# Kernel optimization log

Hardware: AMD Instinct MI355X
Metric: run time of the kernel (lower is better)

## Reference

```python
import jax, jax.numpy as jnp
import numpy as np

K = 32  # knn neighborhood size (hard-coded in get_graph_feature)
EPS_BN = 1e-5


def _bn(x, g, b):
    # batch-norm (training-mode batch stats) over all axes except the last (channel) axis
    axes = tuple(range(x.ndim - 1))
    m = jnp.mean(x, axis=axes, keepdims=True)
    v = jnp.var(x, axis=axes, keepdims=True)
    return (x - m) * jax.lax.rsqrt(v + EPS_BN) * g + b


def _knn_idx(xt, k):
    # xt: [B, N, C] -> indices of k nearest points [B, N, k] (torch topk on -||xi-xj||^2)
    xx = jnp.sum(xt * xt, axis=-1)                       # [B, N]
    inner = jnp.einsum('bnc,bmc->bnm', xt, xt)           # [B, N, N]
    neg_d2 = -(xx[:, :, None] - 2.0 * inner + xx[:, None, :])
    _, idx = jax.lax.top_k(neg_d2, k)
    return idx


def _graph_feature(x, k=K):
    # x: [B, C, N] -> feature [B, N, k, 2C] matching torch cat((neighbors, center))
    xt = jnp.transpose(x, (0, 2, 1))                     # [B, N, C]
    idx = _knn_idx(xt, k)                                # [B, N, k]
    gathered = jax.vmap(lambda a, i: a[i])(xt, idx)      # [B, N, k, C]
    center = jnp.broadcast_to(xt[:, :, None, :], gathered.shape)
    return jnp.concatenate([gathered, center], axis=-1)


def _dgcnn(x, w1, w2, w3, w4, w5, g1, g2, g3, g4, g5, b1, b2, b3, b4, b5):
    # x: [B, 3, N] -> embeddings [B, emb, N]
    feat = _graph_feature(x)                                         # [B, N, K, 6]
    h = jax.nn.relu(_bn(jnp.einsum('bnkc,oc->bnko', feat, w1), g1, b1))
    x1 = jnp.max(h, axis=2)                                          # [B, N, 64]
    h = jax.nn.relu(_bn(jnp.einsum('bnkc,oc->bnko', h, w2), g2, b2))
    x2 = jnp.max(h, axis=2)
    h = jax.nn.relu(_bn(jnp.einsum('bnkc,oc->bnko', h, w3), g3, b3))
    x3 = jnp.max(h, axis=2)
    h = jax.nn.relu(_bn(jnp.einsum('bnkc,oc->bnko', h, w4), g4, b4))
    x4 = jnp.max(h, axis=2)
    cat = jnp.concatenate([x1, x2, x3, x4], axis=-1)                 # [B, N, 512]
    emb = jax.nn.relu(_bn(jnp.einsum('bnc,oc->bno', cat, w5), g5, b5))
    return jnp.transpose(emb, (0, 2, 1))                             # [B, emb, N]


def _pairwise_distance_batch(x, y):
    # x: [B, c, N], y: [B, c, M] -> euclidean distances [B, N, M] (faithful incl. clamp/mask)
    xx = jnp.sum(x * x, axis=1)                          # [B, N]
    yy = jnp.sum(y * y, axis=1)                          # [B, M]
    inner = jnp.einsum('bcn,bcm->bnm', x, y)
    pd = xx[:, :, None] - 2.0 * inner + yy[:, None, :]
    pd_sq = jnp.where(pd > 0.0, pd, 0.0)
    err = (pd_sq <= 0.0).astype(pd.dtype)
    d = jnp.sqrt(pd_sq + err * 1e-16)
    return d * (1.0 - err)


def setup_inputs() -> dict:
    key = jax.random.key(0)
    ks = jax.random.split(key, 20)
    B, N = 4, 2048
    def w(k, o, i):
        return jax.random.normal(k, (o, i), jnp.float32) * (1.0 / np.sqrt(i))
    inp = {
        'src': jax.random.normal(ks[0], (B, 3, N), jnp.float32),
        'tgt': jax.random.normal(ks[1], (B, 3, N), jnp.float32),
        'w1': w(ks[2], 64, 6), 'w2': w(ks[3], 64, 64), 'w3': w(ks[4], 128, 64),
        'w4': w(ks[5], 256, 128), 'w5': w(ks[6], 512, 512),
        'g1': jnp.ones(64), 'g2': jnp.ones(64), 'g3': jnp.ones(128),
        'g4': jnp.ones(256), 'g5': jnp.ones(512),
        'b1': jnp.zeros(64), 'b2': jnp.zeros(64), 'b3': jnp.zeros(128),
        'b4': jnp.zeros(256), 'b5': jnp.zeros(512),
    }
    return inp


def reference(src, tgt, w1, w2, w3, w4, w5, g1, g2, g3, g4, g5, b1, b2, b3, b4, b5):
    params = (w1, w2, w3, w4, w5, g1, g2, g3, g4, g5, b1, b2, b3, b4, b5)
    f_src = _dgcnn(src, *params)                         # [B, emb, N]
    f_tgt = _dgcnn(tgt, *params)                         # [B, emb, N] (siamese)
    d = _pairwise_distance_batch(f_src, f_tgt)           # [B, N, M]
    scores = jax.nn.softmax(-d, axis=-1)                 # soft correspondence
    src_corr = jnp.einsum('bcm,bnm->bcn', tgt, scores)   # tgt @ scores^T, [B, 3, N]
    return src_corr
```

## Files before the change

kernel.cpp:

```cpp
#include <hip/hip_runtime.h>
#include <hip/hip_bf16.h>
#include <math.h>

#define BB 4
#define NN 2048
#define KK 32
#define GG 2
constexpr int BNr = BB * NN;
constexpr int SGr = BB * NN * KK;
constexpr int SR  = GG * SGr;

typedef __hip_bfloat16 bf16;
typedef __attribute__((ext_vector_type(8))) short bf16x8;
typedef __attribute__((ext_vector_type(4))) short s16x4;
typedef __attribute__((ext_vector_type(4))) float f32x4;
__device__ __forceinline__ float b2f(bf16 v) { return __bfloat162float(v); }
__device__ __forceinline__ bf16  f2b(float v) { return __float2bfloat16(v); }
__device__ __forceinline__ short f2bs(float v) { bf16 b = f2b(v); return *(short*)&b; }
__device__ __forceinline__ float bs2f(short s) { bf16 b; *(short*)&b = s; return b2f(b); }

#define SWZ128(b) ((b) ^ ((((b) >> 7) & 7) << 4))
#define SWZ256(b) ((b) ^ ((((b) >> 8) & 7) << 4))

__global__ __launch_bounds__(256) void knn_kernel(const float* __restrict__ src,
                                                  const float* __restrict__ tgt,
                                                  int* __restrict__ idx_out) {
    __shared__ float pts[3 * NN];
    __shared__ float xxs[NN];
    int blk = blockIdx.x;
    int gb = blk >> 9;
    int chunk = blk & 511;
    int g = gb >> 2, b = gb & 3;
    const float* x = (g == 0 ? src : tgt) + (size_t)b * 3 * NN;
    int t = threadIdx.x;
    for (int i = t; i < 3 * NN; i += 256) pts[i] = x[i];
    __syncthreads();
    for (int m = t; m < NN; m += 256) {
        float p0 = pts[m], p1 = pts[NN + m], p2 = pts[2 * NN + m];
        xxs[m] = p0 * p0 + p1 * p1 + p2 * p2;
    }
    __syncthreads();
    int w = t >> 6, l = t & 63;
    int n = chunk * 4 + w;
    float q0 = pts[n], q1 = pts[NN + n], q2 = pts[2 * NN + n];
    float xxn = xxs[n];
    float d2[32];
#pragma unroll
    for (int s = 0; s < 32; ++s) {
        int m = s * 64 + l;
        float dot = q0 * pts[m] + q1 * pts[NN + m] + q2 * pts[2 * NN + m];
        d2[s] = (xxn - 2.0f * dot) + xxs[m];
    }
    float gval[4]; int gslot[4];
#pragma unroll
    for (int G = 0; G < 4; ++G) {
        float v = d2[G * 8]; int sl = G * 8;
#pragma unroll
        for (int s = 1; s < 8; ++s)
            if (d2[G * 8 + s] < v) { v = d2[G * 8 + s]; sl = G * 8 + s; }
        gval[G] = v; gslot[G] = sl;
    }
    int* outp = idx_out + ((size_t)gb * NN + n) * KK;
    for (int k = 0; k < KK; ++k) {
        float bv = fminf(fminf(gval[0], gval[1]), fminf(gval[2], gval[3]));
        float gv = bv;
#pragma unroll
        for (int off = 1; off < 64; off <<= 1) gv = fminf(gv, __shfl_xor(gv, off));
        unsigned long long mask = __ballot(bv == gv);
        int winner = (int)__builtin_ctzll(mask);
        if (l == winner) {
            int grp = (gval[0] == gv) ? 0 : (gval[1] == gv) ? 1 : (gval[2] == gv) ? 2 : 3;
#pragma unroll
            for (int G = 0; G < 4; ++G)
                if (G == grp) {
                    int bs = gslot[G];
                    outp[k] = bs * 64 + l;
#pragma unroll
                    for (int s = 0; s < 8; ++s)
                        if (G * 8 + s == bs) d2[G * 8 + s] = INFINITY;
                    float v = d2[G * 8]; int sl = G * 8;
#pragma unroll
                    for (int s = 1; s < 8; ++s)
                        if (d2[G * 8 + s] < v) { v = d2[G * 8 + s]; sl = G * 8 + s; }
                    gval[G] = v; gslot[G] = sl;
                }
        }
    }
}

__global__ void zero_kernel(float* __restrict__ p, int n) {
    int i = blockIdx.x * 256 + threadIdx.x;
    if (i < n) p[i] = 0.f;
}

__global__ void cvt_all_kernel(const float* __restrict__ w2, const float* __restrict__ w3,
                               const float* __restrict__ w4, const float* __restrict__ w5,
                               bf16* __restrict__ w2b, bf16* __restrict__ w3b,
                               bf16* __restrict__ w4b, bf16* __restrict__ w5b) {
    int i = blockIdx.x * 256 + threadIdx.x;
    if (i < 4096)   w2b[i] = f2b(w2[i]);
    if (i < 8192)   w3b[i] = f2b(w3[i]);
    if (i < 32768)  w4b[i] = f2b(w4[i]);
    if (i < 262144) w5b[i] = f2b(w5[i]);
}

__global__ void finalize_bn_kernel(float* __restrict__ sums, int C,
                                   const float* __restrict__ gamma,
                                   const float* __restrict__ beta,
                                   float cnt, float* __restrict__ params) {
    int i = blockIdx.x * blockDim.x + threadIdx.x;
    if (i >= GG * C) return;
    int g = i / C, c = i - g * C;
    float s  = sums[(g * 512 + c) * 2 + 0];
    float sq = sums[(g * 512 + c) * 2 + 1];
    float mean = s / cnt;
    float var = sq / cnt - mean * mean;
    if (var < 0.f) var = 0.f;
    float sc = gamma[c] * rsqrtf(var + 1e-5f);
    params[(g * 512 + c) * 2 + 0] = sc;
    params[(g * 512 + c) * 2 + 1] = beta[c] - mean * sc;
    sums[(g * 512 + c) * 2 + 0] = 0.f;
    sums[(g * 512 + c) * 2 + 1] = 0.f;
}

template <int MODE>
__global__ __launch_bounds__(256, 3) void l12_mfma(
    const float* __restrict__ src, const float* __restrict__ tgt,
    const float* __restrict__ w1, const bf16* __restrict__ w2b,
    const int* __restrict__ idx, const float* __restrict__ p1,
    bf16* __restrict__ H2, bf16* __restrict__ cat, float* __restrict__ sums) {
    __shared__ char F1s[32768];
    __shared__ char W2s[8192];
    __shared__ float epiA[512];
    __shared__ float epiB[128];
    int tid = threadIdx.x;
    int w = tid >> 6, l = tid & 63, lg = l >> 4, lr = l & 15;
    long long row0 = (long long)blockIdx.x * 256;
    int g = (int)(row0 / SGr);

    epiA[tid] = 0.f; epiA[tid + 256] = 0.f;
    if (MODE == 1) {
        if (tid < 128) epiB[tid] = 0.f;
        for (int s = tid; s < 512; s += 256)
            *(bf16x8*)(W2s + SWZ128(s * 16)) = *(const bf16x8*)(w2b + s * 8);
    }

    bf16x8 af[4];
#pragma unroll
    for (int i = 0; i < 4; ++i) {
        af[i] = (bf16x8){0, 0, 0, 0, 0, 0, 0, 0};
        if (lg == 0) {
            int rr = (int)row0 + w * 64 + 16 * i + lr;
            int nrow = rr >> 5;
            int n = nrow & (NN - 1);
            int gb = nrow >> 11;
            int b = gb & 3, gg = gb >> 2;
            const float* x = (gg ? tgt : src) + (size_t)b * 3 * NN;
            int j = idx[rr];
            af[i][0] = f2bs(x[j]);
            af[i][1] = f2bs(x[NN + j]);
            af[i][2] = f2bs(x[2 * NN + j]);
            af[i][3] = f2bs(x[n]);
            af[i][4] = f2bs(x[NN + n]);
            af[i][5] = f2bs(x[2 * NN + n]);
        }
    }
    bf16x8 bf1[4];
#pragma unroll
    for (int j = 0; j < 4; ++j) {
        bf1[j] = (bf16x8){0, 0, 0, 0, 0, 0, 0, 0};
        if (lg == 0) {
            int o = 16 * j + lr;
#pragma unroll
            for (int c = 0; c < 6; ++c) bf1[j][c] = f2bs(w1[o * 6 + c]);
        }
    }

    f32x4 acc1[4][4] = {};
#pragma unroll
    for (int i = 0; i < 4; ++i)
#pragma unroll
        for (int j = 0; j < 4; ++j)
            acc1[i][j] = __builtin_amdgcn_mfma_f32_16x16x32_bf16(af[i], bf1[j], acc1[i][j], 0, 0, 0);

    __syncthreads();

    if (MODE == 0) {
#pragma unroll
        for (int j = 0; j < 4; ++j) {
            int c = 16 * j + lr;
            float s = 0.f, q = 0.f;
#pragma unroll
            for (int i = 0; i < 4; ++i)
#pragma unroll
                for (int r = 0; r < 4; ++r) { float v = acc1[i][j][r]; s += v; q += v * v; }
            s += __shfl_xor(s, 16); s += __shfl_xor(s, 32);
            q += __shfl_xor(q, 16); q += __shfl_xor(q, 32);
            if (lg == 0) {
                atomicAdd(&epiA[c * 2], s);
                atomicAdd(&epiA[c * 2 + 1], q);
            }
        }
        __syncthreads();
        if (tid < 128) atomicAdd(&sums[g * 1024 + tid], epiA[tid]);
        return;
    }

#pragma unroll
    for (int j = 0; j < 4; ++j) {
        int c = 16 * j + lr;
        float sc = p1[(g * 512 + c) * 2], sh = p1[(g * 512 + c) * 2 + 1];
#pragma unroll
        for (int i = 0; i < 4; ++i) {
            float m = 0.f;
#pragma unroll
            for (int r = 0; r < 4; ++r) {
                float v = fmaf(acc1[i][j][r], sc, sh);
                v = v > 0.f ? v : 0.f;
                m = fmaxf(m, v);
                int rowi = w * 64 + 16 * i + 4 * lg + r;
                *(bf16*)(F1s + SWZ128((rowi * 64 + c) * 2)) = f2b(v);
            }
            int p = 2 * w + (i >> 1);
            atomicMax((int*)epiA + p * 64 + c, __float_as_int(m));
        }
    }
    __syncthreads();

    {
        long long pt0 = row0 >> 5;
        for (int e = tid; e < 512; e += 256) {
            int p = e >> 6, c = e & 63;
            cat[(pt0 + p) * 512 + c] = f2b(__int_as_float(((int*)epiA)[p * 64 + c]));
        }
    }

    f32x4 acc2[4][4] = {};
#pragma unroll
    for (int ks = 0; ks < 2; ++ks) {
        bf16x8 bv[4];
#pragma unroll
        for (int j = 0; j < 4; ++j)
            bv[j] = *(bf16x8*)(W2s + SWZ128(((16 * j + lr) * 64 + ks * 32 + lg * 8) * 2));
#pragma unroll
        for (int i = 0; i < 4; ++i) {
            bf16x8 a = *(bf16x8*)(F1s + SWZ128(((w * 64 + 16 * i + lr) * 64 + ks * 32 + lg * 8) * 2));
#pragma unroll
            for (int j = 0; j < 4; ++j)
                acc2[i][j] = __builtin_amdgcn_mfma_f32_16x16x32_bf16(a, bv[j], acc2[i][j], 0, 0, 0);
        }
    }

#pragma unroll
    for (int j = 0; j < 4; ++j) {
        int c = 16 * j + lr;
        float s = 0.f, q = 0.f;
#pragma unroll
        for (int i = 0; i < 4; ++i)
#pragma unroll
            for (int r = 0; r < 4; ++r) {
                float v = acc2[i][j][r];
                s += v; q += v * v;
                long long gr = row0 + w * 64 + 16 * i + 4 * lg + r;
                H2[gr * 64 + c] = f2b(v);
            }
        s += __shfl_xor(s, 16); s += __shfl_xor(s, 32);
        q += __shfl_xor(q, 16); q += __shfl_xor(q, 32);
        if (lg == 0) {
            atomicAdd(&epiB[c * 2], s);
            atomicAdd(&epiB[c * 2 + 1], q);
        }
    }
    __syncthreads();
    if (tid < 128) atomicAdd(&sums[g * 1024 + tid], epiB[tid]);
}

template <int APPLY>
__global__ __launch_bounds__(512, 2) void chain34_mfma(
    const bf16* __restrict__ H2, const bf16* __restrict__ w3b,
    const bf16* __restrict__ w4b, const float* __restrict__ p2,
    const float* __restrict__ p3, const float* __restrict__ p4,
    bf16* __restrict__ cat, float* __restrict__ sums) {
    extern __shared__ char smem[];
    char* W3s = smem;
    char* W4s = smem + 16384;
    char* A2s = smem + 81920;
    char* F3s = smem + 98304;
    float* P3s = (float*)(smem + 131072);
    float* P4s = (float*)(smem + 132096);
    float* epi = (float*)(smem + 134144);
    float* P2s = (float*)(smem + 138240);

    int tid = threadIdx.x;
    int w = tid >> 6, l = tid & 63, lg = l >> 4, lr = l & 15;
    long long rowB0 = (long long)blockIdx.x * 512;
    int g = (int)(rowB0 / SGr);

    for (int s = tid; s < 1024; s += 512)
        *(bf16x8*)(W3s + SWZ128(s * 16)) = *(const bf16x8*)(w3b + s * 8);
    for (int s = tid; s < 4096; s += 512)
        *(bf16x8*)(W4s + SWZ256(s * 16)) = *(const bf16x8*)(w4b + s * 8);
    if (tid < 256) P3s[tid] = p3[g * 1024 + tid];
    if (tid < 128) P2s[tid] = p2[g * 1024 + tid];
    P4s[tid] = p4 ? p4[g * 1024 + tid] : 0.f;
    if (!APPLY) epi[tid] = 0.f;
    __syncthreads();

    float sc3[4], sh3[4];
#pragma unroll
    for (int r = 0; r < 4; ++r) {
        int c = 16 * w + 4 * lg + r;
        sc3[r] = P3s[c * 2]; sh3[r] = P3s[c * 2 + 1];
    }

    for (int chunk = 0; chunk < 4; ++chunk) {
        long long row0 = rowB0 + chunk * 128;
        for (int s = tid; s < 1024; s += 512) {
            bf16x8 rv = *(const bf16x8*)(H2 + row0 * 64 + s * 8);
            int cb = (s & 7) * 8;
            bf16x8 ov;
#pragma unroll
            for (int e = 0; e < 8; ++e) {
                float v = fmaf(bs2f(rv[e]), P2s[(cb + e) * 2], P2s[(cb + e) * 2 + 1]);
                v = v > 0.f ? v : 0.f;
                ov[e] = f2bs(v);
            }
            *(bf16x8*)(A2s + SWZ128(s * 16)) = ov;
        }
        if (APPLY) { ((int*)epi)[tid] = 0; ((int*)epi)[tid + 512] = 0; }
        __syncthreads();

        {
            f32x4 acc3[8] = {};
#pragma unroll
            for (int ks = 0; ks < 2; ++ks) {
                bf16x8 wf = *(bf16x8*)(W3s + SWZ128(((16 * w + lr) * 64 + ks * 32 + lg * 8) * 2));
#pragma unroll
                for (int j = 0; j < 8; ++j) {
                    bf16x8 a2 = *(bf16x8*)(A2s + SWZ128(((16 * j + lr) * 64 + ks * 32 + lg * 8) * 2));
                    acc3[j] = __builtin_amdgcn_mfma_f32_16x16x32_bf16(wf, a2, acc3[j], 0, 0, 0);
                }
            }
#pragma unroll
            for (int j = 0; j < 8; ++j) {
                s16x4 pk;
#pragma unroll
                for (int r = 0; r < 4; ++r) {
                    float v = fmaf(acc3[j][r], sc3[r], sh3[r]);
                    v = v > 0.f ? v : 0.f;
                    pk[r] = f2bs(v);
                }
                *(s16x4*)(F3s + SWZ256(((16 * j + lr) * 128 + 16 * w + 4 * lg) * 2)) = pk;
            }
        }
        __syncthreads();

        f32x4 acc4[16] = {};
#pragma unroll
        for (int ks = 0; ks < 4; ++ks) {
            bf16x8 a = *(bf16x8*)(F3s + SWZ256(((16 * w + lr) * 128 + ks * 32 + lg * 8) * 2));
#pragma unroll
            for (int j = 0; j < 16; ++j) {
                bf16x8 b = *(bf16x8*)(W4s + SWZ256(((16 * j + lr) * 128 + ks * 32 + lg * 8) * 2));
                acc4[j] = __builtin_amdgcn_mfma_f32_16x16x32_bf16(a, b, acc4[j], 0, 0, 0);
            }
        }

        if (!APPLY) {
#pragma unroll
            for (int j = 0; j < 16; ++j) {
                int c = 16 * j + lr;
                float s = acc4[j][0] + acc4[j][1] + acc4[j][2] + acc4[j][3];
                float q = acc4[j][0] * acc4[j][0] + acc4[j][1] * acc4[j][1] +
                          acc4[j][2] * acc4[j][2] + acc4[j][3] * acc4[j][3];
                s += __shfl_xor(s, 16); s += __shfl_xor(s, 32);
                q += __shfl_xor(q, 16); q += __shfl_xor(q, 32);
                if (lg == 0) {
                    atomicAdd(&epi[c * 2], s);
                    atomicAdd(&epi[c * 2 + 1], q);
                }
            }
        } else {
#pragma unroll
            for (int j = 0; j < 16; ++j) {
                int c = 16 * j + lr;
                float sc = P4s[c * 2], sh = P4s[c * 2 + 1];
                float m = 0.f;
#pragma unroll
                for (int r = 0; r < 4; ++r) {
                    float v = fmaf(acc4[j][r], sc, sh);
                    v = v > 0.f ? v : 0.f;
                    m = fmaxf(m, v);
                }
                m = fmaxf(m, __shfl_xor(m, 16));
                m = fmaxf(m, __shfl_xor(m, 32));
                if (lg == 0)
                    atomicMax((int*)epi + (w >> 1) * 256 + c, __float_as_int(m));
            }
            __syncthreads();
            long long pt0 = row0 >> 5;
            for (int e = tid; e < 1024; e += 512) {
                int p = e >> 8, c = e & 255;
                cat[(pt0 + p) * 512 + 256 + c] = f2b(__int_as_float(((int*)epi)[p * 256 + c]));
            }
            {
                int p = tid >> 7, c = tid & 127;
                float m = 0.f;
                for (int r = 0; r < 32; ++r)
                    m = fmaxf(m, b2f(*(bf16*)(F3s + SWZ256(((p * 32 + r) * 128 + c) * 2))));
                cat[(pt0 + p) * 512 + 128 + c] = f2b(m);
            }
        }
        __syncthreads();
    }
    if (!APPLY) {
        atomicAdd(&sums[g * 1024 + tid], epi[tid]);
    }
}

template <int MODE, int CH, int BNA>
__global__ __launch_bounds__(256, 4) void mfma_gemm(
    const bf16* __restrict__ A, const bf16* __restrict__ Wt,
    float* __restrict__ OutF, bf16* __restrict__ OutB,
    int Cin, int ldOut, long long sA, long long sW, long long sO,
    int rowsPerGroup, const float* __restrict__ params, float* __restrict__ sums,
    const float* __restrict__ pba, bf16* __restrict__ cat) {
    __shared__ char As[16384];
    __shared__ char Bs[8192];
    __shared__ float epi[128];
    __shared__ float PBs[128];
    __shared__ int x2m[256];
    int tid = threadIdx.x;
    int w = tid >> 6, l = tid & 63, lg = l >> 4, lr = l & 15;
    int bz = blockIdx.z;
    const bf16* Ap = A + (long long)bz * sA;
    const bf16* Wp = Wt + (long long)bz * sW;
    int o0 = blockIdx.y * 64;
    long long rowB0 = (long long)blockIdx.x * (128 * CH);
    int g = (int)(rowB0 / rowsPerGroup);
    if ((MODE == 1 || MODE == 3) && tid < 128) epi[tid] = 0.f;
    if (BNA && tid < 128) PBs[tid] = pba[g * 1024 + tid];
    int wr = (w >> 1) * 64, wc = (w & 1) * 32;

    for (int ch = 0; ch < CH; ++ch) {
        long long row0 = rowB0 + (long long)ch * 128;
        if (BNA) {
            __syncthreads();
            if (tid < 256) x2m[tid] = 0;
        }
        f32x4 acc[4][2] = {};
        for (int k0 = 0; k0 < Cin; k0 += 64) {
            __syncthreads();
            for (int s = tid; s < 1024; s += 256) {
                if (BNA) {
                    bf16x8 rv = *(const bf16x8*)(Ap + (row0 + (s >> 3)) * Cin + k0 + (s & 7) * 8);
                    int cb = k0 + (s & 7) * 8;
                    int pt = (s >> 3) >> 5;
                    bf16x8 ov;
#pragma unroll
                    for (int e = 0; e < 8; ++e) {
                        float v = fmaf(bs2f(rv[e]), PBs[(cb + e) * 2], PBs[(cb + e) * 2 + 1]);
                        v = v > 0.f ? v : 0.f;
                        ov[e] = f2bs(v);
                        atomicMax(&x2m[pt * 64 + cb + e], __float_as_int(v));
                    }
                    *(bf16x8*)(As + SWZ128(s * 16)) = ov;
                } else {
                    *(bf16x8*)(As + SWZ128(s * 16)) =
                        *(const bf16x8*)(Ap + (row0 + (s >> 3)) * Cin + k0 + (s & 7) * 8);
                }
            }
            for (int s = tid; s < 512; s += 256)
                *(bf16x8*)(Bs + SWZ128(s * 16)) =
                    *(const bf16x8*)(Wp + (long long)(o0 + (s >> 3)) * Cin + k0 + (s & 7) * 8);
            __syncthreads();
#pragma unroll
            for (int ks = 0; ks < 2; ++ks) {
                bf16x8 b0 = *(bf16x8*)(Bs + SWZ128(((wc + lr) * 64 + ks * 32 + lg * 8) * 2));
                bf16x8 b1 = *(bf16x8*)(Bs + SWZ128(((wc + 16 + lr) * 64 + ks * 32 + lg * 8) * 2));
#pragma unroll
                for (int i = 0; i < 4; ++i) {
                    bf16x8 a = *(bf16x8*)(As + SWZ128(((wr + 16 * i + lr) * 64 + ks * 32 + lg * 8) * 2));
                    acc[i][0] = __builtin_amdgcn_mfma_f32_16x16x32_bf16(a, b0, acc[i][0], 0, 0, 0);
                    acc[i][1] = __builtin_amdgcn_mfma_f32_16x16x32_bf16(a, b1, acc[i][1], 0, 0, 0);
                }
            }
        }
        if (BNA && blockIdx.y == 0) {
            long long pt0 = row0 >> 5;
            if (tid < 256) {
                int p = tid >> 6, c = tid & 63;
                cat[(pt0 + p) * 512 + 64 + c] = f2b(__int_as_float(x2m[tid]));
            }
        }
        if (MODE == 1 || MODE == 3) {
#pragma unroll
            for (int j = 0; j < 2; ++j) {
                int c = wc + 16 * j + lr;
                float s = 0.f, q = 0.f;
#pragma unroll
                for (int i = 0; i < 4; ++i)
#pragma unroll
                    for (int r = 0; r < 4; ++r) {
                        float v = acc[i][j][r];
                        s += v; q += v * v;
                    }
                s += __shfl_xor(s, 16); s += __shfl_xor(s, 32);
                q += __shfl_xor(q, 16); q += __shfl_xor(q, 32);
                if (lg == 0) {
                    atomicAdd(&epi[c * 2], s);
                    atomicAdd(&epi[c * 2 + 1], q);
                }
            }
        }
        if (MODE == 0 || MODE == 3) {
            float* Op = OutF + (long long)bz * sO;
#pragma unroll
            for (int j = 0; j < 2; ++j) {
                int gc = o0 + wc + 16 * j + lr;
#pragma unroll
                for (int i = 0; i < 4; ++i)
#pragma unroll
                    for (int r = 0; r < 4; ++r) {
                        long long gr = row0 + wr + 16 * i + 4 * lg + r;
                        Op[gr * ldOut + gc] = acc[i][j][r];
                    }
            }
        }
    }
    if (MODE == 1 || MODE == 3) {
        __syncthreads();
        if (tid < 128) atomicAdd(&sums[g * 1024 + o0 * 2 + tid], epi[tid]);
    }
}

__global__ __launch_bounds__(256) void emb_finalize(const float* __restrict__ h5,
                                                    const float* __restrict__ p5,
                                                    bf16* __restrict__ embB,
                                                    float* __restrict__ nrm) {
    __shared__ float red[256];
    int row = blockIdx.x; int t = threadIdx.x;
    int g = row / BNr;
    float s = 0.f;
#pragma unroll
    for (int i = 0; i < 2; ++i) {
        int c = t + i * 256;
        float v = fmaf(h5[(size_t)row * 512 + c], p5[(g * 512 + c) * 2], p5[(g * 512 + c) * 2 + 1]);
        v = v > 0.f ? v : 0.f;
        bf16 bb = f2b(v);
        embB[(size_t)row * 512 + c] = bb;
        float vb = b2f(bb);
        s += vb * vb;
    }
    red[t] = s; __syncthreads();
    for (int st = 128; st > 0; st >>= 1) { if (t < st) red[t] += red[t + st]; __syncthreads(); }
    if (t == 0) nrm[row] = red[0];
}

__global__ __launch_bounds__(256) void corr_kernel(const float* __restrict__ inner,
                                                   const float* __restrict__ nrm,
                                                   const float* __restrict__ tgt,
                                                   float* __restrict__ out) {
    __shared__ float red[256];
    int blk = blockIdx.x;
    int b = blk >> 11, n = blk & (NN - 1);
    int t = threadIdx.x;
    const float* inr = inner + ((size_t)b * NN + n) * NN;
    float xx = nrm[b * NN + n];
    float dloc[8];
    float vmax = -INFINITY;
#pragma unroll
    for (int i = 0; i < 8; ++i) {
        int m = t + i * 256;
        float pd = (xx - 2.f * inr[m]) + nrm[BNr + b * NN + m];
        float d = pd > 0.f ? sqrtf(pd) : 0.f;
        dloc[i] = d;
        vmax = fmaxf(vmax, -d);
    }
    red[t] = vmax; __syncthreads();
    for (int s = 128; s > 0; s >>= 1) { if (t < s) red[t] = fmaxf(red[t], red[t + s]); __syncthreads(); }
    vmax = red[0]; __syncthreads();
    const float* tp = tgt + (size_t)b * 3 * NN;
    float se = 0.f, s0 = 0.f, s1 = 0.f, s2 = 0.f;
#pragma unroll
    for (int i = 0; i < 8; ++i) {
        int m = t + i * 256;
        float p = expf(-dloc[i] - vmax);
        se += p;
        s0 += p * tp[m]; s1 += p * tp[NN + m]; s2 += p * tp[2 * NN + m];
    }
    red[t] = se; __syncthreads();
    for (int s = 128; s > 0; s >>= 1) { if (t < s) red[t] += red[t + s]; __syncthreads(); }
    float tot = red[0]; __syncthreads();
    red[t] = s0; __syncthreads();
    for (int s = 128; s > 0; s >>= 1) { if (t < s) red[t] += red[t + s]; __syncthreads(); }
    float o0v = red[0]; __syncthreads();
    red[t] = s1; __syncthreads();
    for (int s = 128; s > 0; s >>= 1) { if (t < s) red[t] += red[t + s]; __syncthreads(); }
    float o1v = red[0]; __syncthreads();
    red[t] = s2; __syncthreads();
    for (int s = 128; s > 0; s >>= 1) { if (t < s) red[t] += red[t + s]; __syncthreads(); }
    float o2v = red[0];
    if (t == 0) {
        out[(size_t)b * 3 * NN + n]          = o0v / tot;
        out[(size_t)b * 3 * NN + NN + n]     = o1v / tot;
        out[(size_t)b * 3 * NN + 2 * NN + n] = o2v / tot;
    }
}

extern "C" void kernel_launch(void* const* d_in, const int* in_sizes, int n_in,
                              void* d_out, int out_size, void* d_ws, size_t ws_size,
                              hipStream_t stream) {
    const float* src = (const float*)d_in[0];
    const float* tgt = (const float*)d_in[1];
    const float* w1  = (const float*)d_in[2];
    const float* w2  = (const float*)d_in[3];
    const float* w3  = (const float*)d_in[4];
    const float* w4  = (const float*)d_in[5];
    const float* w5  = (const float*)d_in[6];
    const float* g1  = (const float*)d_in[7];
    const float* g2  = (const float*)d_in[8];
    const float* g3  = (const float*)d_in[9];
    const float* g4  = (const float*)d_in[10];
    const float* g5  = (const float*)d_in[11];
    const float* b1  = (const float*)d_in[12];
    const float* b2  = (const float*)d_in[13];
    const float* b3  = (const float*)d_in[14];
    const float* b4  = (const float*)d_in[15];
    const float* b5  = (const float*)d_in[16];
    float* out = (float*)d_out;
    char* ws = (char*)d_ws;
    (void)in_sizes; (void)n_in;

    size_t off = 0;
    auto alloc = [&](size_t bytes) { size_t o = off; off = (off + bytes + 255) & ~(size_t)255; return o; };
    int*   idx  = (int*)(ws + alloc((size_t)SR * 4));
    bf16*  H2   = (bf16*)(ws + alloc((size_t)SR * 64 * 2));
    bf16*  cat  = (bf16*)(ws + alloc((size_t)GG * BNr * 512 * 2));
    bf16*  embB = (bf16*)(ws + alloc((size_t)GG * BNr * 512 * 2));
    float* h5   = (float*)(ws + alloc((size_t)GG * BNr * 512 * 4));
    float* nrm  = (float*)(ws + alloc((size_t)GG * BNr * 4));
    float* sums = (float*)(ws + alloc(2048 * 4));
    float* prm  = (float*)(ws + alloc(5 * 2048 * 4));
    bf16*  w2b  = (bf16*)(ws + alloc(4096 * 2));
    bf16*  w3b  = (bf16*)(ws + alloc(8192 * 2));
    bf16*  w4b  = (bf16*)(ws + alloc(32768 * 2));
    bf16*  w5b  = (bf16*)(ws + alloc(262144 * 2));
    float* P1 = prm, *P2 = prm + 2048, *P3 = prm + 4096, *P4 = prm + 6144, *P5 = prm + 8192;
    float* inner = (float*)H2;

    if (ws_size < off) {
        hipMemsetAsync(d_out, 0, (size_t)out_size * 4, stream);
        return;
    }

    knn_kernel<<<GG * BB * NN / 4, 256, 0, stream>>>(src, tgt, idx);
    cvt_all_kernel<<<1024, 256, 0, stream>>>(w2, w3, w4, w5, w2b, w3b, w4b, w5b);
    zero_kernel<<<8, 256, 0, stream>>>(sums, 2048);

    l12_mfma<0><<<SR / 256, 256, 0, stream>>>(src, tgt, w1, w2b, idx, nullptr, nullptr, nullptr, sums);
    finalize_bn_kernel<<<1, 128, 0, stream>>>(sums, 64, g1, b1, (float)SGr, P1);

    l12_mfma<1><<<SR / 256, 256, 0, stream>>>(src, tgt, w1, w2b, idx, P1, H2, cat, sums);
    finalize_bn_kernel<<<1, 128, 0, stream>>>(sums, 64, g2, b2, (float)SGr, P2);

    mfma_gemm<1, 4, 1><<<dim3(SR / 512, 2, 1), 256, 0, stream>>>(
        H2, w3b, nullptr, nullptr, 64, 0, 0, 0, 0, SGr, nullptr, sums, P2, cat);
    finalize_bn_kernel<<<2, 128, 0, stream>>>(sums, 128, g3, b3, (float)SGr, P3);

    chain34_mfma<0><<<1024, 512, 138752, stream>>>(H2, w3b, w4b, P2, P3, nullptr, nullptr, sums);
    finalize_bn_kernel<<<4, 128, 0, stream>>>(sums, 256, g4, b4, (float)SGr, P4);
    chain34_mfma<1><<<1024, 512, 138752, stream>>>(H2, w3b, w4b, P2, P3, P4, cat, nullptr);

    mfma_gemm<3, 1, 0><<<dim3(GG * BNr / 128, 8, 1), 256, 0, stream>>>(
        cat, w5b, h5, nullptr, 512, 512, 0, 0, 0, BNr, nullptr, sums, nullptr, nullptr);
    finalize_bn_kernel<<<8, 128, 0, stream>>>(sums, 512, g5, b5, (float)BNr, P5);
    emb_finalize<<<GG * BNr, 256, 0, stream>>>(h5, P5, embB, nrm);

    mfma_gemm<0, 1, 0><<<dim3(NN / 128, NN / 64, BB), 256, 0, stream>>>(
        embB, embB + (size_t)BNr * 512, inner, nullptr, 512, 2048,
        (long long)NN * 512, (long long)NN * 512, (long long)NN * NN,
        SGr, nullptr, nullptr, nullptr, nullptr);

    corr_kernel<<<BB * NN, 256, 0, stream>>>(inner, nrm, tgt, out);
}
```

Baseline: 697.8 us.

## Compute layer-1 BN stats from input moments in knn; pipeline chain34 loads

Layer-1 BN statistics are now built analytically: the knn kernel accumulates a 27-entry second-moment matrix of the neighbour and centre coordinates, and a new finalize kernel turns it into the per-channel mean and variance through w1. This removes a full l12_mfma pass over all SR rows. chain34 is also restructured: the next H2 chunk is prefetched into registers, the W4/F3 operand roles are swapped so statistics and max reductions stay in registers instead of going through shared-memory atomics, and the epilogue is simplified. The risks are fp32 cancellation in the moment-based variance and extra atomics at the end of knn.

```diff
diff --git a/kernel.cpp b/kernel.cpp
--- a/kernel.cpp
+++ b/kernel.cpp
@@ -24,15 +24,19 @@
 
 __global__ __launch_bounds__(256) void knn_kernel(const float* __restrict__ src,
                                                   const float* __restrict__ tgt,
-                                                  int* __restrict__ idx_out) {
+                                                  int* __restrict__ idx_out,
+                                                  float* __restrict__ g1s) {
     __shared__ float pts[3 * NN];
     __shared__ float xxs[NN];
+    __shared__ int   sel[4][32];
+    __shared__ float Gs[27];
     int blk = blockIdx.x;
     int gb = blk >> 9;
     int chunk = blk & 511;
     int g = gb >> 2, b = gb & 3;
     const float* x = (g == 0 ? src : tgt) + (size_t)b * 3 * NN;
     int t = threadIdx.x;
+    if (t < 27) Gs[t] = 0.f;
     for (int i = t; i < 3 * NN; i += 256) pts[i] = x[i];
     __syncthreads();
     for (int m = t; m < NN; m += 256) {
@@ -75,6 +79,7 @@
                 if (G == grp) {
                     int bs = gslot[G];
                     outp[k] = bs * 64 + l;
+                    sel[w][k] = bs * 64 + l;
 #pragma unroll
                     for (int s = 0; s < 8; ++s)
                         if (G * 8 + s == bs) d2[G * 8 + s] = INFINITY;
@@ -86,6 +91,42 @@
                 }
         }
     }
+    __syncthreads();
+    float nx = 0.f, ny = 0.f, nz = 0.f;
+    if (l < 32) {
+        int m = sel[w][l];
+        nx = pts[m]; ny = pts[NN + m]; nz = pts[2 * NN + m];
+    }
+    float v9[9] = {nx * nx, nx * ny, nx * nz, ny * ny, ny * nz, nz * nz, nx, ny, nz};
+#pragma unroll
+    for (int e = 0; e < 9; ++e) {
+#pragma unroll
+        for (int off = 1; off < 64; off <<= 1) v9[e] += __shfl_xor(v9[e], off);
+    }
+    if (l == 0) {
+        float c3[3] = {q0, q1, q2};
+#pragma unroll
+        for (int e = 0; e < 6; ++e) atomicAdd(&Gs[e], v9[e]);
+#pragma unroll
+        for (int a = 0; a < 3; ++a)
+#pragma unroll
+            for (int bb = 0; bb < 3; ++bb)
+                atomicAdd(&Gs[6 + a * 3 + bb], v9[6 + a] * c3[bb]);
+        atomicAdd(&Gs[15], 32.f * q0 * q0);
+        atomicAdd(&Gs[16], 32.f * q0 * q1);
+        atomicAdd(&Gs[17], 32.f * q0 * q2);
+        atomicAdd(&Gs[18], 32.f * q1 * q1);
+        atomicAdd(&Gs[19], 32.f * q1 * q2);
+        atomicAdd(&Gs[20], 32.f * q2 * q2);
+        atomicAdd(&Gs[21], v9[6]);
+        atomicAdd(&Gs[22], v9[7]);
+        atomicAdd(&Gs[23], v9[8]);
+        atomicAdd(&Gs[24], 32.f * q0);
+        atomicAdd(&Gs[25], 32.f * q1);
+        atomicAdd(&Gs[26], 32.f * q2);
+    }
+    __syncthreads();
+    if (t < 27) atomicAdd(&g1s[g * 27 + t], Gs[t]);
 }
 
 __global__ void zero_kernel(float* __restrict__ p, int n) {
@@ -123,7 +164,36 @@
     sums[(g * 512 + c) * 2 + 1] = 0.f;
 }
 
-template <int MODE>
+__global__ void finalize_l1_kernel(const float* __restrict__ g1s,
+                                   const float* __restrict__ w1,
+                                   const float* __restrict__ gamma,
+                                   const float* __restrict__ beta,
+                                   float cnt, float* __restrict__ params) {
+    int i = blockIdx.x * blockDim.x + threadIdx.x;
+    if (i >= GG * 64) return;
+    int g = i >> 6, o = i & 63;
+    const float* G = g1s + g * 27;
+    float wv[6];
+#pragma unroll
+    for (int c = 0; c < 6; ++c) wv[c] = w1[o * 6 + c];
+    float s = wv[0] * G[21] + wv[1] * G[22] + wv[2] * G[23] +
+              wv[3] * G[24] + wv[4] * G[25] + wv[5] * G[26];
+    const int UT[6][6] = {{0, 1, 2, 6, 7, 8},   {1, 3, 4, 9, 10, 11},
+                          {2, 4, 5, 12, 13, 14},{6, 9, 12, 15, 16, 17},
+                          {7, 10, 13, 16, 18, 19},{8, 11, 14, 17, 19, 20}};
+    float q = 0.f;
+#pragma unroll
+    for (int a = 0; a < 6; ++a)
+#pragma unroll
+        for (int bb = 0; bb < 6; ++bb) q += wv[a] * wv[bb] * G[UT[a][bb]];
+    float mean = s / cnt;
+    float var = q / cnt - mean * mean;
+    if (var < 0.f) var = 0.f;
+    float sc = gamma[o] * rsqrtf(var + 1e-5f);
+    params[(g * 512 + o) * 2 + 0] = sc;
+    params[(g * 512 + o) * 2 + 1] = beta[o] - mean * sc;
+}
+
 __global__ __launch_bounds__(256, 3) void l12_mfma(
     const float* __restrict__ src, const float* __restrict__ tgt,
     const float* __restrict__ w1, const bf16* __restrict__ w2b,
@@ -139,11 +209,9 @@
     int g = (int)(row0 / SGr);
 
     epiA[tid] = 0.f; epiA[tid + 256] = 0.f;
-    if (MODE == 1) {
-        if (tid < 128) epiB[tid] = 0.f;
-        for (int s = tid; s < 512; s += 256)
-            *(bf16x8*)(W2s + SWZ128(s * 16)) = *(const bf16x8*)(w2b + s * 8);
-    }
+    if (tid < 128) epiB[tid] = 0.f;
+    for (int s = tid; s < 512; s += 256)
+        *(bf16x8*)(W2s + SWZ128(s * 16)) = *(const bf16x8*)(w2b + s * 8);
 
     bf16x8 af[4];
 #pragma unroll
@@ -185,27 +253,6 @@
 
     __syncthreads();
 
-    if (MODE == 0) {
-#pragma unroll
-        for (int j = 0; j < 4; ++j) {
-            int c = 16 * j + lr;
-            float s = 0.f, q = 0.f;
-#pragma unroll
-            for (int i = 0; i < 4; ++i)
-#pragma unroll
-                for (int r = 0; r < 4; ++r) { float v = acc1[i][j][r]; s += v; q += v * v; }
-            s += __shfl_xor(s, 16); s += __shfl_xor(s, 32);
-            q += __shfl_xor(q, 16); q += __shfl_xor(q, 32);
-            if (lg == 0) {
-                atomicAdd(&epiA[c * 2], s);
-                atomicAdd(&epiA[c * 2 + 1], q);
-            }
-        }
-        __syncthreads();
-        if (tid < 128) atomicAdd(&sums[g * 1024 + tid], epiA[tid]);
-        return;
-    }
-
 #pragma unroll
     for (int j = 0; j < 4; ++j) {
         int c = 16 * j + lr;
@@ -303,7 +350,9 @@
     if (tid < 256) P3s[tid] = p3[g * 1024 + tid];
     if (tid < 128) P2s[tid] = p2[g * 1024 + tid];
     P4s[tid] = p4 ? p4[g * 1024 + tid] : 0.f;
-    if (!APPLY) epi[tid] = 0.f;
+
+    bf16x8 rv0 = *(const bf16x8*)(H2 + rowB0 * 64 + (long long)tid * 8);
+    bf16x8 rv1 = *(const bf16x8*)(H2 + rowB0 * 64 + (long long)(tid + 512) * 8);
     __syncthreads();
 
     float sc3[4], sh3[4];
@@ -312,24 +361,34 @@
         int c = 16 * w + 4 * lg + r;
         sc3[r] = P3s[c * 2]; sh3[r] = P3s[c * 2 + 1];
     }
+    float sc4[2][4], sh4[2][4];
+    if (APPLY) {
+#pragma unroll
+        for (int i = 0; i < 2; ++i)
+#pragma unroll
+            for (int r = 0; r < 4; ++r) {
+                int c = 16 * (2 * w + i) + 4 * lg + r;
+                sc4[i][r] = P4s[c * 2]; sh4[i][r] = P4s[c * 2 + 1];
+            }
+    }
+    float sacc[2][4] = {}, qacc[2][4] = {};
+
+    auto bn2w = [&](bf16x8 rv, int s) {
+        int cb = (s & 7) * 8;
+        bf16x8 ov;
+#pragma unroll
+        for (int e = 0; e < 8; ++e) {
+            float v = fmaf(bs2f(rv[e]), P2s[(cb + e) * 2], P2s[(cb + e) * 2 + 1]);
+            v = v > 0.f ? v : 0.f;
+            ov[e] = f2bs(v);
+        }
+        *(bf16x8*)(A2s + SWZ128(s * 16)) = ov;
+    };
+    bn2w(rv0, tid); bn2w(rv1, tid + 512);
+    __syncthreads();
 
     for (int chunk = 0; chunk < 4; ++chunk) {
         long long row0 = rowB0 + chunk * 128;
-        for (int s = tid; s < 1024; s += 512) {
-            bf16x8 rv = *(const bf16x8*)(H2 + row0 * 64 + s * 8);
-            int cb = (s & 7) * 8;
-            bf16x8 ov;
-#pragma unroll
-            for (int e = 0; e < 8; ++e) {
-                float v = fmaf(bs2f(rv[e]), P2s[(cb + e) * 2], P2s[(cb + e) * 2 + 1]);
-                v = v > 0.f ? v : 0.f;
-                ov[e] = f2bs(v);
-            }
-            *(bf16x8*)(A2s + SWZ128(s * 16)) = ov;
-        }
-        if (APPLY) { ((int*)epi)[tid] = 0; ((int*)epi)[tid + 512] = 0; }
-        __syncthreads();
-
         {
             f32x4 acc3[8] = {};
 #pragma unroll
@@ -353,55 +412,65 @@
                 *(s16x4*)(F3s + SWZ256(((16 * j + lr) * 128 + 16 * w + 4 * lg) * 2)) = pk;
             }
         }
+        if (chunk < 3) {
+            long long rn = rowB0 + (chunk + 1) * 128;
+            rv0 = *(const bf16x8*)(H2 + rn * 64 + (long long)tid * 8);
+            rv1 = *(const bf16x8*)(H2 + rn * 64 + (long long)(tid + 512) * 8);
+        }
         __syncthreads();
 
-        f32x4 acc4[16] = {};
+        f32x4 acc4[2][8] = {};
 #pragma unroll
         for (int ks = 0; ks < 4; ++ks) {
-            bf16x8 a = *(bf16x8*)(F3s + SWZ256(((16 * w + lr) * 128 + ks * 32 + lg * 8) * 2));
-#pragma unroll
-            for (int j = 0; j < 16; ++j) {
-                bf16x8 b = *(bf16x8*)(W4s + SWZ256(((16 * j + lr) * 128 + ks * 32 + lg * 8) * 2));
-                acc4[j] = __builtin_amdgcn_mfma_f32_16x16x32_bf16(a, b, acc4[j], 0, 0, 0);
+            bf16x8 a0 = *(bf16x8*)(W4s + SWZ256(((16 * (2 * w) + lr) * 128 + ks * 32 + lg * 8) * 2));
+            bf16x8 a1 = *(bf16x8*)(W4s + SWZ256(((16 * (2 * w + 1) + lr) * 128 + ks * 32 + lg * 8) * 2));
+#pragma unroll
+            for (int j = 0; j < 8; ++j) {
+                bf16x8 bfr = *(bf16x8*)(F3s + SWZ256(((16 * j + lr) * 128 + ks * 32 + lg * 8) * 2));
+                acc4[0][j] = __builtin_amdgcn_mfma_f32_16x16x32_bf16(a0, bfr, acc4[0][j], 0, 0, 0);
+                acc4[1][j] = __builtin_amdgcn_mfma_f32_16x16x32_bf16(a1, bfr, acc4[1][j], 0, 0, 0);
             }
         }
 
         if (!APPLY) {
 #pragma unroll
-            for (int j = 0; j < 16; ++j) {
-                int c = 16 * j + lr;
-                float s = acc4[j][0] + acc4[j][1] + acc4[j][2] + acc4[j][3];
-                float q = acc4[j][0] * acc4[j][0] + acc4[j][1] * acc4[j][1] +
-                          acc4[j][2] * acc4[j][2] + acc4[j][3] * acc4[j][3];
-                s += __shfl_xor(s, 16); s += __shfl_xor(s, 32);
-                q += __shfl_xor(q, 16); q += __shfl_xor(q, 32);
-                if (lg == 0) {
-                    atomicAdd(&epi[c * 2], s);
-                    atomicAdd(&epi[c * 2 + 1], q);
-                }
-            }
+            for (int i = 0; i < 2; ++i)
+#pragma unroll
+                for (int r = 0; r < 4; ++r) {
+                    float s = 0.f, q = 0.f;
+#pragma unroll
+                    for (int j = 0; j < 8; ++j) {
+                        float v = acc4[i][j][r];
+                        s += v; q += v * v;
+                    }
+                    sacc[i][r] += s; qacc[i][r] += q;
+                }
         } else {
 #pragma unroll
-            for (int j = 0; j < 16; ++j) {
-                int c = 16 * j + lr;
-                float sc = P4s[c * 2], sh = P4s[c * 2 + 1];
-                float m = 0.f;
+            for (int i = 0; i < 2; ++i)
 #pragma unroll
                 for (int r = 0; r < 4; ++r) {
-                    float v = fmaf(acc4[j][r], sc, sh);
-                    v = v > 0.f ? v : 0.f;
-                    m = fmaxf(m, v);
-                }
-                m = fmaxf(m, __shfl_xor(m, 16));
-                m = fmaxf(m, __shfl_xor(m, 32));
-                if (lg == 0)
-                    atomicMax((int*)epi + (w >> 1) * 256 + c, __float_as_int(m));
-            }
+                    float sc = sc4[i][r], sh = sh4[i][r];
+#pragma unroll
+                    for (int p = 0; p < 4; ++p) {
+                        float v0 = fmaf(acc4[i][2 * p][r], sc, sh);
+                        float v1 = fmaf(acc4[i][2 * p + 1][r], sc, sh);
+                        v0 = v0 > 0.f ? v0 : 0.f;
+                        v1 = v1 > 0.f ? v1 : 0.f;
+                        float m = fmaxf(v0, v1);
+                        m = fmaxf(m, __shfl_xor(m, 1));
+                        m = fmaxf(m, __shfl_xor(m, 2));
+                        m = fmaxf(m, __shfl_xor(m, 4));
+                        m = fmaxf(m, __shfl_xor(m, 8));
+                        if (lr == 0)
+                            epi[p * 256 + 16 * (2 * w + i) + 4 * lg + r] = m;
+                    }
+                }
             __syncthreads();
             long long pt0 = row0 >> 5;
             for (int e = tid; e < 1024; e += 512) {
                 int p = e >> 8, c = e & 255;
-                cat[(pt0 + p) * 512 + 256 + c] = f2b(__int_as_float(((int*)epi)[p * 256 + c]));
+                cat[(pt0 + p) * 512 + 256 + c] = f2b(epi[e]);
             }
             {
                 int p = tid >> 7, c = tid & 127;
@@ -412,9 +481,27 @@
             }
         }
         __syncthreads();
+        if (chunk < 3) {
+            bn2w(rv0, tid); bn2w(rv1, tid + 512);
+            __syncthreads();
+        }
     }
     if (!APPLY) {
-        atomicAdd(&sums[g * 1024 + tid], epi[tid]);
+#pragma unroll
+        for (int i = 0; i < 2; ++i)
+#pragma unroll
+            for (int r = 0; r < 4; ++r) {
+                float s = sacc[i][r], q = qacc[i][r];
+                s += __shfl_xor(s, 1); s += __shfl_xor(s, 2);
+                s += __shfl_xor(s, 4); s += __shfl_xor(s, 8);
+                q += __shfl_xor(q, 1); q += __shfl_xor(q, 2);
+                q += __shfl_xor(q, 4); q += __shfl_xor(q, 8);
+                if (lr == 0) {
+                    int c = 16 * (2 * w + i) + 4 * lg + r;
+                    atomicAdd(&sums[g * 1024 + c * 2], s);
+                    atomicAdd(&sums[g * 1024 + c * 2 + 1], q);
+                }
+            }
     }
 }
 
@@ -641,6 +728,7 @@
     float* h5   = (float*)(ws + alloc((size_t)GG * BNr * 512 * 4));
     float* nrm  = (float*)(ws + alloc((size_t)GG * BNr * 4));
     float* sums = (float*)(ws + alloc(2048 * 4));
+    float* g1s  = (float*)(ws + alloc(64 * 4));
     float* prm  = (float*)(ws + alloc(5 * 2048 * 4));
     bf16*  w2b  = (bf16*)(ws + alloc(4096 * 2));
     bf16*  w3b  = (bf16*)(ws + alloc(8192 * 2));
@@ -654,14 +742,13 @@
         return;
     }
 
-    knn_kernel<<<GG * BB * NN / 4, 256, 0, stream>>>(src, tgt, idx);
+    zero_kernel<<<9, 256, 0, stream>>>(sums, 2048 + 64);
+    knn_kernel<<<GG * BB * NN / 4, 256, 0, stream>>>(src, tgt, idx, g1s);
     cvt_all_kernel<<<1024, 256, 0, stream>>>(w2, w3, w4, w5, w2b, w3b, w4b, w5b);
-    zero_kernel<<<8, 256, 0, stream>>>(sums, 2048);
-
-    l12_mfma<0><<<SR / 256, 256, 0, stream>>>(src, tgt, w1, w2b, idx, nullptr, nullptr, nullptr, sums);
-    finalize_bn_kernel<<<1, 128, 0, stream>>>(sums, 64, g1, b1, (float)SGr, P1);
-
-    l12_mfma<1><<<SR / 256, 256, 0, stream>>>(src, tgt, w1, w2b, idx, P1, H2, cat, sums);
+
+    finalize_l1_kernel<<<1, 128, 0, stream>>>(g1s, w1, g1, b1, (float)SGr, P1);
+
+    l12_mfma<<<SR / 256, 256, 0, stream>>>(src, tgt, w1, w2b, idx, P1, H2, cat, sums);
     finalize_bn_kernel<<<1, 128, 0, stream>>>(sums, 64, g2, b2, (float)SGr, P2);
 
     mfma_gemm<1, 4, 1><<<dim3(SR / 512, 2, 1), 256, 0, stream>>>(
```

After: 718.3 us. +2.9%, slower.
